# Performance work log

Hardware: AMD Instinct MI355X
Metric: run time of the kernel (lower is better)

The kernel has to match this reference:

```python
import jax
import jax.numpy as jnp
import numpy as np

LATENT = 4096
LABEL = 512
CLUSTERING_N = 1

# Sign with straight-through gradient (matches torch Sign.backward = identity)
@jax.custom_vjp
def sign_ste(x):
    return (x >= 0).astype(x.dtype) * 2 - 1

def _sign_fwd(x):
    return sign_ste(x), None

def _sign_bwd(_, g):
    return (g,)

sign_ste.defvjp(_sign_fwd, _sign_bwd)

# MaxOneHot: keep only argmax entry; backward passes 0.5*grad at argmax
@jax.custom_vjp
def max_onehot(x):
    idx = jnp.argmax(x)
    return jnp.zeros_like(x).at[idx].set(x[idx])

def _moh_fwd(x):
    idx = jnp.argmax(x)
    return jnp.zeros_like(x).at[idx].set(x[idx]), idx

def _moh_bwd(idx, g):
    return (0.5 * jnp.zeros_like(g).at[idx].set(g[idx]),)

max_onehot.defvjp(_moh_fwd, _moh_bwd)


def setup_inputs() -> dict:
    key = jax.random.key(0)
    k1, k2 = jax.random.split(key)
    s = jax.random.normal(k1, (LATENT,), dtype=jnp.float32)
    # matches torch init: 2*rand - 1 in (-1, 1)
    llv = 2.0 * jax.random.uniform(k2, (LABEL, LATENT), dtype=jnp.float32) - 1.0
    return {"s": s, "label_latent_vectors": llv}


def _hopfield_forward(s, llv):
    # weight build: x = sign(clamp(llv)); W = sum_i outer(x_i - rho) / label_size, zero diag
    x = sign_ste(jnp.clip(llv, -1.0, 1.0))          # [LABEL, LATENT]
    rho = jnp.mean(x)
    temp = x - rho                                   # [LABEL, LATENT]
    weight = (temp.T @ temp) / jnp.asarray(x.shape[0], x.dtype)  # [LATENT, LATENT]
    weight = weight - jnp.diag(jnp.diag(weight))

    # Gauss-Seidel sweep: sequential update s[i] = sign(W[i] . stop_grad(s))
    def step(s_carry, wi_i):
        wi, i = wi_i
        v = jnp.dot(wi, jax.lax.stop_gradient(s_carry))
        return s_carry.at[i].set(sign_ste(v)), None

    idxs = jnp.arange(weight.shape[0])
    for _ in range(CLUSTERING_N):
        s, _ = jax.lax.scan(step, s, (weight, idxs))

    scores = jnp.abs(s @ x.T) / jnp.asarray(s.shape[0], s.dtype)  # [LABEL]
    return max_onehot(scores)


def reference(s, label_latent_vectors):
    return _hopfield_forward(s, label_latent_vectors)
```

## Files before the change

### kernel.cpp

```cpp
#include <hip/hip_runtime.h>
#include <hip/hip_bf16.h>


#define OFF_COLB   0u
#define OFF_XBITS  (256u<<10)
#define OFF_XBW    (512u<<10)
#define OFF_KF     (768u<<10)
#define OFF_BCORR  (1792u<<10)
#define OFF_U      (1808u<<10)
#define OFF_CST    (1936u<<10)
#define OFF_P0     (2000u<<10)
#define OFF_SBITS  (2002u<<10)
#define OFF_CNT    (2003u<<10)
#define OFF_HDR    (2019u<<10)
#define OFF_BS0    (2020u<<10)
#define OFF_BS0C   (2021u<<10)

template<int CTRL, int RMASK>
__device__ __forceinline__ float dpp_add(float x){
  int t = __builtin_amdgcn_update_dpp(0, __float_as_int(x), CTRL, RMASK, 0xf, true);
  return x + __int_as_float(t);
}
__device__ __forceinline__ float wave_allsum(float x){
  x = dpp_add<0x111,0xf>(x);
  x = dpp_add<0x112,0xf>(x);
  x = dpp_add<0x114,0xf>(x);
  x = dpp_add<0x118,0xf>(x);
  x = dpp_add<0x142,0xa>(x);
  x = dpp_add<0x143,0xc>(x);
  return __int_as_float(__builtin_amdgcn_readlane(__float_as_int(x), 63));
}

__global__ void k_xbits(const float* __restrict__ llv, unsigned long long* __restrict__ xbits,
                        unsigned long long* __restrict__ xbitsW){
  int w = threadIdx.x >> 6, lane = threadIdx.x & 63;
  int l = blockIdx.x*4 + w;
  unsigned long long myword = 0;
  for (int c = 0; c < 64; ++c){
    float v = llv[(size_t)l*4096 + c*64 + lane];
    unsigned long long b = __ballot(v >= 0.0f);
    if (c == lane) myword = b;
  }
  xbits[(size_t)l*64 + lane] = myword;
  xbitsW[(size_t)lane*512 + l] = myword;
}

__global__ void k_bitT(const unsigned long long* __restrict__ xbits,
                       unsigned long long* __restrict__ colbitsP){
  int li = blockIdx.x, ii = blockIdx.y, lane = threadIdx.x;
  unsigned long long w = xbits[(size_t)(li*64 + lane)*64 + ii];
  unsigned long long myw = 0;
  for (int j = 0; j < 64; ++j){
    unsigned long long b = __ballot((w >> j) & 1ull);
    if (j == lane) myw = b;
  }
  colbitsP[(size_t)li*4096 + ii*64 + lane] = myw;
}

__global__ void k_colc(const unsigned long long* __restrict__ colbitsP, int* __restrict__ colcnt){
  int i = blockIdx.x*256 + threadIdx.x;
  int c = 0;
  #pragma unroll
  for (int wl = 0; wl < 8; ++wl) c += __popcll(colbitsP[(size_t)wl*4096 + i]);
  colcnt[i] = c;
}

__global__ void k_rho(const int* __restrict__ colcnt, float* __restrict__ hdr){
  __shared__ int sh[256];
  int tid = threadIdx.x;
  int s = 0;
  for (int k = tid; k < 4096; k += 256) s += colcnt[k];
  sh[tid] = s; __syncthreads();
  for (int st = 128; st > 0; st >>= 1){
    if (tid < st) sh[tid] += sh[tid + st];
    __syncthreads();
  }
  if (tid == 0){
    int num = 2*sh[0] - 2097152;
    hdr[0] = (float)num * (1.0f/2097152.0f);
  }
}

__global__ void k_const(const int* __restrict__ colcnt, const float* __restrict__ hdr,
                        const float* __restrict__ s0, float4* __restrict__ cst){
  int i = blockIdx.x*256 + threadIdx.x;
  float rho = hdr[0];
  float c  = (float)(2*colcnt[i] - 512);
  float r2 = rho*rho;
  float q  = 512.0f + 512.0f*r2 - 2.0f*rho*c;
  float s  = s0[i];
  float4 o;
  o.x = q * s;
  o.y = rho*c - 512.0f*r2;
  o.z = 1.0f - s;
  o.w = c;
  cst[i] = o;
}

__global__ void k_kdiag(const unsigned long long* __restrict__ colbitsP,
                        const float4* __restrict__ cst, const float* __restrict__ s0,
                        const float* __restrict__ hdr,
                        float* __restrict__ Kf, float* __restrict__ baseCorr,
                        float* __restrict__ blkS0, float* __restrict__ blkS0C){
  __shared__ unsigned long long cb[8][64];
  __shared__ float Kl[64][64];
  __shared__ float cs[64], ss[64];
  int b = blockIdx.x, i0 = b*64, tid = threadIdx.x;
  for (int k = tid; k < 512; k += 256)
    cb[k>>6][k&63] = colbitsP[(size_t)(k>>6)*4096 + i0 + (k&63)];
  if (tid < 64){ cs[tid] = cst[i0+tid].w; ss[tid] = s0[i0+tid]; }
  __syncthreads();
  float rho = hdr[0];
  float r2t = 512.0f*rho*rho;
  #pragma unroll
  for (int k = 0; k < 16; ++k){
    int q = tid*16 + k;
    int t = q >> 6, j = q & 63;
    int acc = 0;
    #pragma unroll
    for (int wl = 0; wl < 8; ++wl) acc += __popcll(cb[wl][t] ^ cb[wl][j]);
    float G = (float)(512 - 2*acc);
    float kf = G - rho*(cs[t]+cs[j]) + r2t;
    Kl[t][j] = kf;
    Kf[(size_t)b*4096 + q] = kf;
  }
  __syncthreads();
  if (tid < 64){
    float bc = 0.0f;
    for (int j = 0; j < tid; ++j) bc = fmaf(ss[j], Kl[tid][j], bc);
    baseCorr[i0 + tid] = bc;
  }
  if (tid == 64){
    float a = 0.0f, b2 = 0.0f;
    for (int j = 0; j < 64; ++j){ a += ss[j]; b2 = fmaf(ss[j], cs[j], b2); }
    blkS0[b] = a; blkS0C[b] = b2;
  }
}

__global__ void k_u(const unsigned long long* __restrict__ xbits, const float* __restrict__ s0,
                    float* __restrict__ U){
  __shared__ float s0l[64];
  int b = blockIdx.x, l = threadIdx.x;
  if (l < 64) s0l[l] = s0[b*64 + l];
  __syncthreads();
  unsigned long long w = xbits[(size_t)l*64 + b];
  unsigned int lo = (unsigned)w, hi = (unsigned)(w >> 32);
  unsigned int nlo = ~lo, nhi = ~hi;
  float acc = 0.0f;
  #pragma unroll
  for (int j = 0; j < 32; ++j){
    unsigned int m = (nlo << (31-j)) & 0x80000000u;
    acc += __uint_as_float(__float_as_uint(s0l[j]) ^ m);
  }
  #pragma unroll
  for (int j = 0; j < 32; ++j){
    unsigned int m = (nhi << (31-j)) & 0x80000000u;
    acc += __uint_as_float(__float_as_uint(s0l[32+j]) ^ m);
  }
  U[(size_t)b*512 + l] = acc;
}

__global__ void k_pinit(const float* __restrict__ llv, const float* __restrict__ s0,
                        float* __restrict__ p0){
  int l = blockIdx.x, lane = threadIdx.x;
  float acc = 0.0f;
  for (int c = 0; c < 64; ++c){
    float v = llv[(size_t)l*4096 + c*64 + lane];
    float sg = (v >= 0.0f) ? 1.0f : -1.0f;
    acc = fmaf(sg, s0[c*64 + lane], acc);
  }
  float tot = wave_allsum(acc);
  if (lane == 0) p0[l] = tot;
}

#define ACC1(F, W, JS) { \
  unsigned int m_ = ((~(W)) << (31-(JS))) & 0x80000000u; \
  acc += __uint_as_float(__float_as_uint(F) ^ m_); }

#define BSTP(KVAL, J) { \
  unsigned long long neg_ = __ballot(__float_as_int(v) < 0); \
  unsigned b_ = (unsigned)(neg_ >> (J)) & 1u; \
  sg_ |= ((unsigned long long)(b_ ^ 1u)) << (J); \
  v = v + __uint_as_float(__float_as_uint(KVAL) ^ (b_ << 31)); }
#define BST4(Q, J0) BSTP(Q.x,(J0)+0) BSTP(Q.y,(J0)+1) BSTP(Q.z,(J0)+2) BSTP(Q.w,(J0)+3)

__global__ __launch_bounds__(512, 1)
void k_sweep6(const unsigned long long* __restrict__ colbitsP,
              const unsigned long long* __restrict__ xbitsW,
              const float* __restrict__ Kf, const float* __restrict__ baseCorr,
              const float* __restrict__ blkS0, const float* __restrict__ blkS0C,
              const float* __restrict__ U, const float4* __restrict__ cst,
              const float* __restrict__ p0, const float* __restrict__ s0,
              const float* __restrict__ hdr, unsigned long long* __restrict__ sbits)
{
  __shared__ float Kl[2][64][64];
  __shared__ unsigned long long cbl[2][8][64];
  __shared__ unsigned long long xbl[2][512];
  __shared__ float Ul[2][512];
  __shared__ float4 cstl[2][64];
  __shared__ float bcl[2][64];
  __shared__ float bs0l[64], bscl[64];
  __shared__ float p[512];
  __shared__ float part[8][64];
  __shared__ float red[512];
  __shared__ unsigned long long sig;

  int tid = threadIdx.x, g = tid >> 6, t = tid & 63;
  float rho = hdr[0];

  p[tid] = p0[tid];
  red[tid] = p0[tid];
  if (tid < 64){ bs0l[tid] = blkS0[tid]; bscl[tid] = blkS0C[tid]; }
  __syncthreads();
  for (int st = 256; st > 0; st >>= 1){ if (tid < st) red[tid] += red[tid+st]; __syncthreads(); }
  float Preg = red[0];
  __syncthreads();
  { float a = 0.0f; for (int k = 0; k < 8; ++k) a += s0[tid*8 + k]; red[tid] = a; }
  __syncthreads();
  for (int st = 256; st > 0; st >>= 1){ if (tid < st) red[tid] += red[tid+st]; __syncthreads(); }
  float Treg = red[0];
  __syncthreads();

  {
    const float4* Ks = (const float4*)(Kf);
    #pragma unroll
    for (int k = 0; k < 4; ++k){
      int e = tid + k*512;
      float4 vv = Ks[e];
      int gie = e >> 10, row = (e >> 4) & 63, f = e & 15;
      *((float4*)&Kl[gie][row][0] + (f ^ (row & 15))) = vv;
    }
    #pragma unroll
    for (int k = 0; k < 2; ++k){
      int e = tid + k*512;
      int run = e >> 6, tt = e & 63, gie = run >> 3, wl = run & 7;
      cbl[gie][wl][tt] = colbitsP[(size_t)wl*4096 + gie*64 + tt];
    }
    #pragma unroll
    for (int k = 0; k < 2; ++k){
      int e = tid + k*512;
      ((unsigned long long*)xbl)[e] = xbitsW[e];
    }
    #pragma unroll
    for (int k = 0; k < 2; ++k){
      int e = tid + k*512;
      ((float*)Ul)[e] = U[e];
    }
    if (tid < 128){
      ((float4*)cstl)[tid] = cst[tid];
      ((float*)bcl)[tid]   = baseCorr[tid];
    }
  }
  __syncthreads();

  for (int grp = 0; grp < 32; ++grp){
    int ng = grp + 1;
    bool pf = (ng < 32);
    float4 kv0, kv1, kv2, kv3, cstv;
    unsigned long long cbv0, cbv1, xbv0, xbv1;
    float uv0, uv1, bcv;
    if (pf){
      const float4* Ks = (const float4*)(Kf + (size_t)ng*8192);
      kv0 = Ks[tid]; kv1 = Ks[tid+512]; kv2 = Ks[tid+1024]; kv3 = Ks[tid+1536];
      { int e = tid;       int run = e>>6, tt = e&63;
        cbv0 = colbitsP[(size_t)(run&7)*4096 + (ng*2 + (run>>3))*64 + tt]; }
      { int e = tid + 512; int run = e>>6, tt = e&63;
        cbv1 = colbitsP[(size_t)(run&7)*4096 + (ng*2 + (run>>3))*64 + tt]; }
      xbv0 = xbitsW[(size_t)ng*1024 + tid]; xbv1 = xbitsW[(size_t)ng*1024 + tid + 512];
      uv0  = U[(size_t)ng*1024 + tid];      uv1  = U[(size_t)ng*1024 + tid + 512];
      if (tid < 128){ cstv = cst[ng*128 + tid]; bcv = baseCorr[ng*128 + tid]; }
    }

    #pragma unroll
    for (int gi = 0; gi < 2; ++gi){
      int b = grp*2 + gi;
      {
        unsigned long long w = cbl[gi][g][t];
        unsigned int lo = (unsigned)w, hi = (unsigned)(w >> 32);
        const float4* pw = (const float4*)(p + g*64);
        float acc = 0.0f;
        #pragma unroll
        for (int f = 0; f < 16; ++f){
          float4 q = pw[f];
          if (f < 8){
            ACC1(q.x, lo, 4*f+0) ACC1(q.y, lo, 4*f+1)
            ACC1(q.z, lo, 4*f+2) ACC1(q.w, lo, 4*f+3)
          } else {
            ACC1(q.x, hi, 4*f-32) ACC1(q.y, hi, 4*f-31)
            ACC1(q.z, hi, 4*f-30) ACC1(q.w, hi, 4*f-29)
          }
        }
        part[g][t] = acc;
      }
      __syncthreads();

      if (g == 0){
        const float4* Kp = (const float4*)&Kl[gi][t][0];
        int sw = t & 15;
        float S = 0.0f;
        #pragma unroll
        for (int gg = 0; gg < 8; ++gg) S += part[gg][t];
        float4 cc = cstl[gi][t];
        float bc_ = bcl[gi][t];
        float v = S - cc.x - rho*Preg - cc.y*Treg - bc_;
        float4 C0 = Kp[0^sw], C1 = Kp[1^sw], C2 = Kp[2^sw];
        unsigned long long sg_ = 0ull;
        BST4(C0, 0);   C0 = Kp[3^sw];
        BST4(C1, 4);   C1 = Kp[4^sw];
        BST4(C2, 8);   C2 = Kp[5^sw];
        BST4(C0, 12);  C0 = Kp[6^sw];
        BST4(C1, 16);  C1 = Kp[7^sw];
        BST4(C2, 20);  C2 = Kp[8^sw];
        BST4(C0, 24);  C0 = Kp[9^sw];
        BST4(C1, 28);  C1 = Kp[10^sw];
        BST4(C2, 32);  C2 = Kp[11^sw];
        BST4(C0, 36);  C0 = Kp[12^sw];
        BST4(C1, 40);  C1 = Kp[13^sw];
        BST4(C2, 44);  C2 = Kp[14^sw];
        BST4(C0, 48);  C0 = Kp[15^sw];
        BST4(C1, 52);
        BST4(C2, 56);
        BST4(C0, 60);
        if (t == 0){ sig = sg_; sbits[b] = sg_; }
        float sv = ((sg_ >> t) & 1ull) ? cc.w : -cc.w;
        float sc = wave_allsum(sv);
        int pcs = __popcll(sg_);
        Preg += sc - bscl[b];
        Treg += (float)(2*pcs - 64) - bs0l[b];
      }
      __syncthreads();
      {
        unsigned long long sgv = sig;
        int pc = __popcll(xbl[gi][tid] ^ sgv);
        p[tid] = p[tid] + (float)(64 - 2*pc) - Ul[gi][tid];
      }
    }

    if (pf){
      { int e = tid;        int gie=e>>10, row=(e>>4)&63, f=e&15;
        *((float4*)&Kl[gie][row][0] + (f ^ (row & 15))) = kv0; }
      { int e = tid + 512;  int gie=e>>10, row=(e>>4)&63, f=e&15;
        *((float4*)&Kl[gie][row][0] + (f ^ (row & 15))) = kv1; }
      { int e = tid + 1024; int gie=e>>10, row=(e>>4)&63, f=e&15;
        *((float4*)&Kl[gie][row][0] + (f ^ (row & 15))) = kv2; }
      { int e = tid + 1536; int gie=e>>10, row=(e>>4)&63, f=e&15;
        *((float4*)&Kl[gie][row][0] + (f ^ (row & 15))) = kv3; }
      { int e = tid;       int run=e>>6, tt=e&63; cbl[run>>3][run&7][tt] = cbv0; }
      { int e = tid + 512; int run=e>>6, tt=e&63; cbl[run>>3][run&7][tt] = cbv1; }
      ((unsigned long long*)xbl)[tid]       = xbv0;
      ((unsigned long long*)xbl)[tid + 512] = xbv1;
      ((float*)Ul)[tid]       = uv0;
      ((float*)Ul)[tid + 512] = uv1;
      if (tid < 128){ ((float4*)cstl)[tid] = cstv; ((float*)bcl)[tid] = bcv; }
    }
    __syncthreads();
  }
}

__global__ void k_scores(const unsigned long long* __restrict__ xbits,
                         const unsigned long long* __restrict__ sbits,
                         float* __restrict__ out){
  __shared__ unsigned long long sb[64];
  __shared__ int bestkey;
  int tid = threadIdx.x;
  if (tid < 64) sb[tid] = sbits[tid];
  if (tid == 0) bestkey = -1;
  __syncthreads();
  int acc = 0;
  #pragma unroll
  for (int w = 0; w < 64; ++w)
    acc += __popcll(xbits[(size_t)tid*64 + w] ^ sb[w]);
  int dot = 4096 - 2*acc;
  int ad  = dot < 0 ? -dot : dot;
  int key = (ad << 10) | (511 - tid);
  atomicMax(&bestkey, key);
  __syncthreads();
  int bl = 511 - (bestkey & 1023);
  float val = (float)(bestkey >> 10) * (1.0f/4096.0f);
  out[tid] = (tid == bl) ? val : 0.0f;
}

extern "C" void kernel_launch(void* const* d_in, const int* in_sizes, int n_in,
                              void* d_out, int out_size, void* d_ws, size_t ws_size,
                              hipStream_t stream){
  const float* s0  = (const float*)d_in[0];
  const float* llv = (const float*)d_in[1];
  float* out = (float*)d_out;
  char* ws = (char*)d_ws;

  unsigned long long* colbitsP = (unsigned long long*)(ws + OFF_COLB);
  unsigned long long* xbits    = (unsigned long long*)(ws + OFF_XBITS);
  unsigned long long* xbitsW   = (unsigned long long*)(ws + OFF_XBW);
  float*  Kf    = (float*)(ws + OFF_KF);
  float*  bcorr = (float*)(ws + OFF_BCORR);
  float*  U     = (float*)(ws + OFF_U);
  float4* cst   = (float4*)(ws + OFF_CST);
  float*  p0    = (float*)(ws + OFF_P0);
  unsigned long long* sbits = (unsigned long long*)(ws + OFF_SBITS);
  int*    colcnt = (int*)(ws + OFF_CNT);
  float*  hdr   = (float*)(ws + OFF_HDR);
  float*  bS0   = (float*)(ws + OFF_BS0);
  float*  bS0C  = (float*)(ws + OFF_BS0C);

  k_xbits<<<128, 256, 0, stream>>>(llv, xbits, xbitsW);
  k_bitT<<<dim3(8, 64), 64, 0, stream>>>(xbits, colbitsP);
  k_colc<<<16, 256, 0, stream>>>(colbitsP, colcnt);
  k_rho<<<1, 256, 0, stream>>>(colcnt, hdr);
  k_const<<<16, 256, 0, stream>>>(colcnt, hdr, s0, cst);
  k_kdiag<<<64, 256, 0, stream>>>(colbitsP, cst, s0, hdr, Kf, bcorr, bS0, bS0C);
  k_u<<<64, 512, 0, stream>>>(xbits, s0, U);
  k_pinit<<<512, 64, 0, stream>>>(llv, s0, p0);
  k_sweep6<<<1, 512, 0, stream>>>(colbitsP, xbitsW, Kf, bcorr, bS0, bS0C, U, cst, p0, s0, hdr, sbits);
  k_scores<<<1, 512, 0, stream>>>(xbits, sbits, out);
}
```

Baseline: 210.8 us.

## Resolve four sequential sign decisions per ballot using DPP quad broadcasts

Replaces the per-element ballot chain in the in-block Gauss-Seidel step (64 serial ballots) with groups of four. Quad-broadcast DPP reads let each lane in a quad compute the corrected value for its position locally, so one ballot settles four sign decisions at a time. This cuts the serial ballot/SALU dependency chain by four times, at the cost of extra DPP moves and VALU work per group. Floating-point summation order changes slightly, which could flip signs near zero.

```diff
diff --git a/kernel.cpp b/kernel.cpp
--- a/kernel.cpp
+++ b/kernel.cpp
@@ -177,12 +177,35 @@
   unsigned int m_ = ((~(W)) << (31-(JS))) & 0x80000000u; \
   acc += __uint_as_float(__float_as_uint(F) ^ m_); }
 
-#define BSTP(KVAL, J) { \
-  unsigned long long neg_ = __ballot(__float_as_int(v) < 0); \
-  unsigned b_ = (unsigned)(neg_ >> (J)) & 1u; \
-  sg_ |= ((unsigned long long)(b_ ^ 1u)) << (J); \
-  v = v + __uint_as_float(__float_as_uint(KVAL) ^ (b_ << 31)); }
-#define BST4(Q, J0) BSTP(Q.x,(J0)+0) BSTP(Q.y,(J0)+1) BSTP(Q.z,(J0)+2) BSTP(Q.w,(J0)+3)
+#define FU(x) __float_as_uint(x)
+#define UF(x) __uint_as_float(x)
+#define QB(SRC, R) __int_as_float(__builtin_amdgcn_update_dpp(0, __float_as_int(SRC), (R)*0x55, 0xf, 0xf, true))
+
+#define GRPQ(CQ, Qi) { \
+  float w0_ = QB(v,0), w1_ = QB(v,1), w2_ = QB(v,2), w3_ = QB(v,3); \
+  float k10_ = QB(CQ.x,1), k20_ = QB(CQ.x,2), k30_ = QB(CQ.x,3); \
+  float k21_ = QB(CQ.y,2), k31_ = QB(CQ.y,3); \
+  float k32_ = QB(CQ.z,3); \
+  unsigned m0_ = FU(w0_) & 0x80000000u; \
+  float u1_ = w1_ + UF(FU(k10_)^m0_); \
+  unsigned m1_ = FU(u1_) & 0x80000000u; \
+  float u2_ = (w2_ + UF(FU(k20_)^m0_)) + UF(FU(k21_)^m1_); \
+  unsigned m2_ = FU(u2_) & 0x80000000u; \
+  float u3_ = ((w3_ + UF(FU(k30_)^m0_)) + UF(FU(k31_)^m1_)) + UF(FU(k32_)^m2_); \
+  float uo_ = (r_ == 0) ? w0_ : (r_ == 1) ? u1_ : (r_ == 2) ? u2_ : u3_; \
+  unsigned long long neg_ = __ballot(__float_as_int(uo_) < 0); \
+  unsigned b0_ = (unsigned)(neg_ >> (4*(Qi)+0)) & 1u; \
+  unsigned b1_ = (unsigned)(neg_ >> (4*(Qi)+1)) & 1u; \
+  unsigned b2_ = (unsigned)(neg_ >> (4*(Qi)+2)) & 1u; \
+  unsigned b3_ = (unsigned)(neg_ >> (4*(Qi)+3)) & 1u; \
+  sg_ |= ((unsigned long long)(b0_^1u)) << (4*(Qi)+0); \
+  sg_ |= ((unsigned long long)(b1_^1u)) << (4*(Qi)+1); \
+  sg_ |= ((unsigned long long)(b2_^1u)) << (4*(Qi)+2); \
+  sg_ |= ((unsigned long long)(b3_^1u)) << (4*(Qi)+3); \
+  float t01_ = UF(FU(CQ.x)^(b0_<<31)) + UF(FU(CQ.y)^(b1_<<31)); \
+  float t23_ = UF(FU(CQ.z)^(b2_<<31)) + UF(FU(CQ.w)^(b3_<<31)); \
+  v = v + (t01_ + t23_); \
+}
 
 __global__ __launch_bounds__(512, 1)
 void k_sweep6(const unsigned long long* __restrict__ colbitsP,
@@ -297,6 +320,7 @@
       if (g == 0){
         const float4* Kp = (const float4*)&Kl[gi][t][0];
         int sw = t & 15;
+        int r_ = t & 3;
         float S = 0.0f;
         #pragma unroll
         for (int gg = 0; gg < 8; ++gg) S += part[gg][t];
@@ -305,22 +329,22 @@
         float v = S - cc.x - rho*Preg - cc.y*Treg - bc_;
         float4 C0 = Kp[0^sw], C1 = Kp[1^sw], C2 = Kp[2^sw];
         unsigned long long sg_ = 0ull;
-        BST4(C0, 0);   C0 = Kp[3^sw];
-        BST4(C1, 4);   C1 = Kp[4^sw];
-        BST4(C2, 8);   C2 = Kp[5^sw];
-        BST4(C0, 12);  C0 = Kp[6^sw];
-        BST4(C1, 16);  C1 = Kp[7^sw];
-        BST4(C2, 20);  C2 = Kp[8^sw];
-        BST4(C0, 24);  C0 = Kp[9^sw];
-        BST4(C1, 28);  C1 = Kp[10^sw];
-        BST4(C2, 32);  C2 = Kp[11^sw];
-        BST4(C0, 36);  C0 = Kp[12^sw];
-        BST4(C1, 40);  C1 = Kp[13^sw];
-        BST4(C2, 44);  C2 = Kp[14^sw];
-        BST4(C0, 48);  C0 = Kp[15^sw];
-        BST4(C1, 52);
-        BST4(C2, 56);
-        BST4(C0, 60);
+        GRPQ(C0, 0);   C0 = Kp[3^sw];
+        GRPQ(C1, 1);   C1 = Kp[4^sw];
+        GRPQ(C2, 2);   C2 = Kp[5^sw];
+        GRPQ(C0, 3);   C0 = Kp[6^sw];
+        GRPQ(C1, 4);   C1 = Kp[7^sw];
+        GRPQ(C2, 5);   C2 = Kp[8^sw];
+        GRPQ(C0, 6);   C0 = Kp[9^sw];
+        GRPQ(C1, 7);   C1 = Kp[10^sw];
+        GRPQ(C2, 8);   C2 = Kp[11^sw];
+        GRPQ(C0, 9);   C0 = Kp[12^sw];
+        GRPQ(C1, 10);  C1 = Kp[13^sw];
+        GRPQ(C2, 11);  C2 = Kp[14^sw];
+        GRPQ(C0, 12);  C0 = Kp[15^sw];
+        GRPQ(C1, 13);
+        GRPQ(C2, 14);
+        GRPQ(C0, 15);
         if (t == 0){ sig = sg_; sbits[b] = sg_; }
         float sv = ((sg_ >> t) & 1ull) ? cc.w : -cc.w;
         float sc = wave_allsum(sv);
```

Result: slower. 238.2 us (+13.0%).
